# Kernel tuning notes

Measured on AMD Instinct MI355X. Metric: run time of the kernel, lower is better.

The kernel has to match this reference:

```python
import jax, jax.numpy as jnp
import numpy as np

N = 100000      # nodes
E = 3200000     # edges (avg degree 32)
F_IN = 11       # QM9 node feature dim
H = 32          # hidden dim (hard-coded in module)
C = 16          # num_classes


def setup_inputs() -> dict:
    key = jax.random.key(0)
    ks = jax.random.split(key, 8)
    x = jax.random.normal(ks[0], (N, F_IN), jnp.float32)
    edge_index = jax.random.randint(ks[1], (2, E), 0, N, dtype=jnp.int32)
    W1 = jax.random.normal(ks[2], (F_IN, H), jnp.float32) / np.sqrt(F_IN)
    b1 = jnp.zeros((H,), jnp.float32)
    W2 = jax.random.normal(ks[3], (H, H), jnp.float32) / np.sqrt(H)
    b2 = jnp.zeros((H,), jnp.float32)
    W3 = jax.random.normal(ks[4], (H, C), jnp.float32) / np.sqrt(H)
    b3 = jnp.zeros((C,), jnp.float32)
    return {"x": x, "edge_index": edge_index, "W1": W1, "b1": b1,
            "W2": W2, "b2": b2, "W3": W3, "b3": b3}


def gcn_conv(x, src, dst, dinv, W, b):
    # PyG GCNConv: x' = D^{-1/2} (A + I) D^{-1/2} (x W) + b
    h = x @ W                                   # [N, out]
    coef = dinv[src] * dinv[dst]                # [E] symmetric norm per edge
    msg = h[src] * coef[:, None]                # gather + scale
    agg = jnp.zeros_like(h).at[dst].add(msg)    # scatter-add to targets
    agg = agg + h * (dinv * dinv)[:, None]      # self-loop contribution
    return agg + b


def reference(x, edge_index, W1, b1, W2, b2, W3, b3):
    src, dst = edge_index[0], edge_index[1]
    n = x.shape[0]
    # degree including self-loop (counted at target node)
    deg = jnp.zeros((n,), x.dtype).at[dst].add(1.0) + 1.0
    dinv = jax.lax.rsqrt(deg)
    h = jax.nn.relu(gcn_conv(x, src, dst, dinv, W1, b1))
    h = jax.nn.relu(gcn_conv(h, src, dst, dinv, W2, b2))
    h = gcn_conv(h, src, dst, dinv, W3, b3)
    return jax.nn.log_softmax(h, axis=1)
```

## Files before the change

### kernel.cpp

```cpp
#include <hip/hip_runtime.h>
#include <hip/hip_bf16.h>

#define FIN 11
#define HD 32
#define NC 16

#define BK_BITS 9
#define BK_NODES 512
#define NB_MAX 196
#define CAPE 18500
#define STAGE_DEPTH 48
#define FLUSH_N 32

using bf16 = __hip_bfloat16;

static __device__ __forceinline__ float b2f(bf16 v) { return __bfloat162float(v); }

static __device__ __forceinline__ unsigned short f2bf_bits(float f) {
    unsigned int x = __float_as_uint(f);
    return (unsigned short)((x + 0x7FFFu + ((x >> 16) & 1u)) >> 16);
}
static __device__ __forceinline__ float bits2f(unsigned short u) {
    return __uint_as_float(((unsigned int)u) << 16);
}

__global__ __launch_bounds__(256) void k_detect(const unsigned int* __restrict__ xw, int* __restrict__ flag,
                                                int* __restrict__ gcur, int nbq) {
    __shared__ int cnt;
    if (threadIdx.x == 0) cnt = 0;
    __syncthreads();
    for (int i = threadIdx.x; i <= nbq; i += 256) gcur[i] = 0;
    int c = 0;
    for (int i = threadIdx.x; i < 1024; i += 256) c += (xw[i] >> 14) & 1;
    atomicAdd(&cnt, c);
    __syncthreads();
    if (threadIdx.x == 0) *flag = (cnt > 256) ? 1 : 0;
}

__global__ __launch_bounds__(256) void k_binA(const int* __restrict__ ei, int ne, int nb, int per,
                                              int* __restrict__ gcur, unsigned int* __restrict__ bout) {
    __shared__ unsigned int stage[NB_MAX][STAGE_DEPTH];
    __shared__ int cnt[NB_MAX];
    for (int i = threadIdx.x; i < nb; i += 256) cnt[i] = 0;
    __syncthreads();
    int e0 = blockIdx.x * per;
    int e1 = min(e0 + per, ne);
    const int* eis = ei;
    const int* eid = ei + ne;
    for (int base = e0; base < e1; base += 1024) {
#pragma unroll
        for (int k = 0; k < 4; k++) {
            int e = base + k * 256 + threadIdx.x;
            if (e < e1) {
                int s = eis[e], d = eid[e];
                int b = d >> BK_BITS;
                unsigned int pk = ((unsigned int)s << BK_BITS) | (unsigned int)(d & (BK_NODES - 1));
                if (b < nb) {
                    int slot = atomicAdd(&cnt[b], 1);
                    if (slot < STAGE_DEPTH) {
                        stage[b][slot] = pk;
                    } else {
                        atomicSub(&cnt[b], 1);
                        int pos = atomicAdd(&gcur[b], 1);
                        if (pos < CAPE) bout[(size_t)b * CAPE + pos] = pk;
                    }
                }
            }
        }
        __syncthreads();
        if (threadIdx.x < (unsigned)nb) {
            int t = threadIdx.x;
            while (cnt[t] >= FLUSH_N) {
                int pos = atomicAdd(&gcur[t], FLUSH_N);
                if (pos + FLUSH_N <= CAPE) {
                    unsigned int* dstp = bout + (size_t)t * CAPE + pos;
#pragma unroll
                    for (int i = 0; i < FLUSH_N; i++) dstp[i] = stage[t][i];
                }
                int rem = cnt[t] - FLUSH_N;
                for (int i = 0; i < rem; i++) stage[t][i] = stage[t][FLUSH_N + i];
                cnt[t] = rem;
            }
        }
        __syncthreads();
    }
    if (threadIdx.x < (unsigned)nb) {
        int t = threadIdx.x;
        int c = cnt[t];
        if (c > 0) {
            int pos = atomicAdd(&gcur[t], c);
            for (int i = 0; i < c; i++)
                if (pos + i < CAPE) bout[(size_t)t * CAPE + pos + i] = stage[t][i];
        }
    }
}

__global__ __launch_bounds__(256) void k_binB(const unsigned int* __restrict__ bout,
                                              const int* __restrict__ gcur,
                                              float* __restrict__ dinv, int* __restrict__ rowptr,
                                              int* __restrict__ csr, int nn, int nb) {
    __shared__ unsigned int csrimg[CAPE];
    __shared__ int hist[BK_NODES];
    __shared__ int cur[BK_NODES];
    __shared__ int sred[256];
    __shared__ int sbase;
    int b = blockIdx.x;
    {
        int accb = 0, acct = 0;
        for (int i = threadIdx.x; i < nb; i += 256) {
            int v = min(gcur[i], CAPE);
            if (i < b) accb += v;
            acct += v;
        }
        sred[threadIdx.x] = accb;
        __syncthreads();
        for (int off = 128; off > 0; off >>= 1) {
            if (threadIdx.x < off) sred[threadIdx.x] += sred[threadIdx.x + off];
            __syncthreads();
        }
        if (threadIdx.x == 0) sbase = sred[0];
        __syncthreads();
        if (b == 0) {
            sred[threadIdx.x] = acct;
            __syncthreads();
            for (int off = 128; off > 0; off >>= 1) {
                if (threadIdx.x < off) sred[threadIdx.x] += sred[threadIdx.x + off];
                __syncthreads();
            }
            if (threadIdx.x == 0) rowptr[nn] = sred[0];
            __syncthreads();
        }
    }
    int n0 = b << BK_BITS;
    int nval = min(BK_NODES, nn - n0);
    int cnt = min(gcur[b], CAPE);
    int base = sbase;
    const unsigned int* src = bout + (size_t)b * CAPE;
    for (int i = threadIdx.x; i < BK_NODES; i += 256) hist[i] = 0;
    __syncthreads();
    for (int i = threadIdx.x; i < cnt; i += 256)
        atomicAdd(&hist[src[i] & (BK_NODES - 1)], 1);
    __syncthreads();
    for (int i = threadIdx.x; i < nval; i += 256)
        dinv[n0 + i] = rsqrtf((float)hist[i] + 1.0f);
    for (int i = threadIdx.x; i < BK_NODES; i += 256) cur[i] = hist[i];
    __syncthreads();
    for (int off = 1; off < BK_NODES; off <<= 1) {
        int i0 = threadIdx.x, i1 = threadIdx.x + 256;
        int v0 = (i0 >= off) ? cur[i0 - off] : 0;
        int v1 = (i1 >= off) ? cur[i1 - off] : 0;
        __syncthreads();
        cur[i0] += v0;
        cur[i1] += v1;
        __syncthreads();
    }
    for (int i = threadIdx.x; i < BK_NODES; i += 256) {
        int excl = cur[i] - hist[i];
        if (i < nval) rowptr[n0 + i] = base + excl;
        cur[i] = excl;
    }
    __syncthreads();
    for (int i = threadIdx.x; i < cnt; i += 256) {
        unsigned int pk = src[i];
        int l = pk & (BK_NODES - 1);
        int pos = atomicAdd(&cur[l], 1);
        if (pos < CAPE) csrimg[pos] = pk >> BK_BITS;
    }
    __syncthreads();
    for (int i = threadIdx.x; i < cnt; i += 256)
        csr[base + i] = (int)csrimg[i];
}

__global__ __launch_bounds__(256) void k_mm1(const void* __restrict__ xv, const void* __restrict__ Wv,
                                             const int* __restrict__ flag, const float* __restrict__ dinv,
                                             unsigned short* __restrict__ hs, int nn) {
    __shared__ float sW[FIN * HD];
    bool f32 = (*flag != 0);
    if (f32) {
        const float* W = (const float*)Wv;
        for (int i = threadIdx.x; i < FIN * HD; i += blockDim.x) sW[i] = W[i];
    } else {
        const bf16* W = (const bf16*)Wv;
        for (int i = threadIdx.x; i < FIN * HD; i += blockDim.x) sW[i] = b2f(W[i]);
    }
    __syncthreads();
    int t = blockIdx.x * blockDim.x + threadIdx.x;
    int n = t >> 5, j = t & 31;
    if (n >= nn) return;
    float xr[FIN];
    if (f32) {
        const float* p = (const float*)xv + (size_t)n * FIN;
#pragma unroll
        for (int k = 0; k < FIN; k++) xr[k] = p[k];
    } else {
        const bf16* p = (const bf16*)xv + (size_t)n * FIN;
#pragma unroll
        for (int k = 0; k < FIN; k++) xr[k] = b2f(p[k]);
    }
    float acc = 0.0f;
#pragma unroll
    for (int k = 0; k < FIN; k++) acc += xr[k] * sW[k * HD + j];
    hs[(size_t)n * HD + j] = f2bf_bits(acc * dinv[n]);
}

__global__ __launch_bounds__(256) void k_mm2(const void* __restrict__ Wv, const int* __restrict__ flag,
                                             const float* __restrict__ dinv, const float* __restrict__ agg,
                                             unsigned short* __restrict__ hs, int nn) {
    __shared__ float sW[HD * HD];
    __shared__ float sIn[8 * HD];
    bool f32 = (*flag != 0);
    if (f32) {
        const float* W = (const float*)Wv;
        for (int i = threadIdx.x; i < HD * HD; i += blockDim.x) sW[i] = W[i];
    } else {
        const bf16* W = (const bf16*)Wv;
        for (int i = threadIdx.x; i < HD * HD; i += blockDim.x) sW[i] = b2f(W[i]);
    }
    int r0 = blockIdx.x * 8;
    {
        size_t idx = (size_t)r0 * HD + threadIdx.x;
        if (idx < (size_t)nn * HD) {
            float v = agg[idx];
            sIn[threadIdx.x] = v > 0.0f ? v : 0.0f;
        }
    }
    __syncthreads();
    int n = r0 + (threadIdx.x >> 5), j = threadIdx.x & 31;
    if (n >= nn) return;
    const float* r = sIn + (threadIdx.x >> 5) * HD;
    float acc = 0.0f;
#pragma unroll
    for (int k = 0; k < HD; k++) acc += r[k] * sW[k * HD + j];
    hs[(size_t)n * HD + j] = f2bf_bits(acc * dinv[n]);
}

__global__ __launch_bounds__(256) void k_mm3(const void* __restrict__ Wv, const int* __restrict__ flag,
                                             const float* __restrict__ dinv, const float* __restrict__ agg,
                                             unsigned short* __restrict__ hs3, int nn) {
    __shared__ float sW[HD * NC];
    __shared__ float sIn[16 * HD];
    bool f32 = (*flag != 0);
    if (f32) {
        const float* W = (const float*)Wv;
        for (int i = threadIdx.x; i < HD * NC; i += blockDim.x) sW[i] = W[i];
    } else {
        const bf16* W = (const bf16*)Wv;
        for (int i = threadIdx.x; i < HD * NC; i += blockDim.x) sW[i] = b2f(W[i]);
    }
    int r0 = blockIdx.x * 16;
#pragma unroll
    for (int u = 0; u < 2; u++) {
        size_t idx = (size_t)r0 * HD + u * 256 + threadIdx.x;
        if (idx < (size_t)nn * HD) {
            float v = agg[idx];
            sIn[u * 256 + threadIdx.x] = v > 0.0f ? v : 0.0f;
        }
    }
    __syncthreads();
    int n = r0 + (threadIdx.x >> 4), j = threadIdx.x & 15;
    if (n >= nn) return;
    const float* r = sIn + (threadIdx.x >> 4) * HD;
    float acc = 0.0f;
#pragma unroll
    for (int k = 0; k < HD; k++) acc += r[k] * sW[k * NC + j];
    hs3[(size_t)n * NC + j] = f2bf_bits(acc * dinv[n]);
}

__global__ __launch_bounds__(256) void k_g32(const int* __restrict__ rowptr, const int* __restrict__ csr,
                                             const float* __restrict__ dinv, const unsigned short* __restrict__ hs,
                                             const void* __restrict__ bv, const int* __restrict__ flag,
                                             float* __restrict__ agg, int nn) {
    __shared__ float sb[HD];
    bool f32 = (*flag != 0);
    if (threadIdx.x < HD)
        sb[threadIdx.x] = f32 ? ((const float*)bv)[threadIdx.x] : b2f(((const bf16*)bv)[threadIdx.x]);
    __syncthreads();
    int node = blockIdx.x * 4 + (threadIdx.x >> 6);
    if (node >= nn) return;
    int lane = threadIdx.x & 63;
    int g = lane >> 3, q = lane & 7;
    int rs = rowptr[node], re = rowptr[node + 1];
    int deg = re - rs;
    float a0 = 0.0f, a1 = 0.0f, a2 = 0.0f, a3 = 0.0f;
    if (g == 0) {
        uint2 hv = *(const uint2*)(hs + (size_t)node * HD + q * 4);
        a0 = bits2f((unsigned short)(hv.x & 0xFFFFu));
        a1 = bits2f((unsigned short)(hv.x >> 16));
        a2 = bits2f((unsigned short)(hv.y & 0xFFFFu));
        a3 = bits2f((unsigned short)(hv.y >> 16));
    }
    for (int k0 = 0; k0 < deg; k0 += 64) {
        int nk = min(64, deg - k0);
        int myidx = (lane < nk) ? csr[rs + k0 + lane] : 0;
        for (int k = g; k < nk; k += 8) {
            int s = __shfl(myidx, k);
            uint2 hv = *(const uint2*)(hs + (size_t)s * HD + q * 4);
            a0 += bits2f((unsigned short)(hv.x & 0xFFFFu));
            a1 += bits2f((unsigned short)(hv.x >> 16));
            a2 += bits2f((unsigned short)(hv.y & 0xFFFFu));
            a3 += bits2f((unsigned short)(hv.y >> 16));
        }
    }
#pragma unroll
    for (int off = 8; off < 64; off <<= 1) {
        a0 += __shfl_xor(a0, off);
        a1 += __shfl_xor(a1, off);
        a2 += __shfl_xor(a2, off);
        a3 += __shfl_xor(a3, off);
    }
    if (g == 0) {
        float di = dinv[node];
        float4 o = make_float4(di * a0 + sb[q * 4 + 0], di * a1 + sb[q * 4 + 1],
                               di * a2 + sb[q * 4 + 2], di * a3 + sb[q * 4 + 3]);
        *(float4*)(agg + (size_t)node * HD + q * 4) = o;
    }
}

__global__ __launch_bounds__(256) void k_g16lsm(const int* __restrict__ rowptr, const int* __restrict__ csr,
                                                const float* __restrict__ dinv, const unsigned short* __restrict__ hs,
                                                const void* __restrict__ bv, const int* __restrict__ flag,
                                                void* __restrict__ outv, int nn) {
    __shared__ float sb[NC];
    bool f32 = (*flag != 0);
    if (threadIdx.x < NC)
        sb[threadIdx.x] = f32 ? ((const float*)bv)[threadIdx.x] : b2f(((const bf16*)bv)[threadIdx.x]);
    __syncthreads();
    int node = blockIdx.x * 4 + (threadIdx.x >> 6);
    if (node >= nn) return;
    int lane = threadIdx.x & 63;
    int g = lane >> 2, q = lane & 3;
    int rs = rowptr[node], re = rowptr[node + 1];
    int deg = re - rs;
    float a0 = 0.0f, a1 = 0.0f, a2 = 0.0f, a3 = 0.0f;
    if (g == 0) {
        uint2 hv = *(const uint2*)(hs + (size_t)node * NC + q * 4);
        a0 = bits2f((unsigned short)(hv.x & 0xFFFFu));
        a1 = bits2f((unsigned short)(hv.x >> 16));
        a2 = bits2f((unsigned short)(hv.y & 0xFFFFu));
        a3 = bits2f((unsigned short)(hv.y >> 16));
    }
    for (int k0 = 0; k0 < deg; k0 += 64) {
        int nk = min(64, deg - k0);
        int myidx = (lane < nk) ? csr[rs + k0 + lane] : 0;
        for (int k = g; k < nk; k += 16) {
            int s = __shfl(myidx, k);
            uint2 hv = *(const uint2*)(hs + (size_t)s * NC + q * 4);
            a0 += bits2f((unsigned short)(hv.x & 0xFFFFu));
            a1 += bits2f((unsigned short)(hv.x >> 16));
            a2 += bits2f((unsigned short)(hv.y & 0xFFFFu));
            a3 += bits2f((unsigned short)(hv.y >> 16));
        }
    }
#pragma unroll
    for (int off = 4; off < 64; off <<= 1) {
        a0 += __shfl_xor(a0, off);
        a1 += __shfl_xor(a1, off);
        a2 += __shfl_xor(a2, off);
        a3 += __shfl_xor(a3, off);
    }
    if (g == 0) {
        float di = dinv[node];
        float v0 = di * a0 + sb[q * 4 + 0];
        float v1 = di * a1 + sb[q * 4 + 1];
        float v2 = di * a2 + sb[q * 4 + 2];
        float v3 = di * a3 + sb[q * 4 + 3];
        float m = fmaxf(fmaxf(v0, v1), fmaxf(v2, v3));
        m = fmaxf(m, __shfl_xor(m, 1));
        m = fmaxf(m, __shfl_xor(m, 2));
        float s = __expf(v0 - m) + __expf(v1 - m) + __expf(v2 - m) + __expf(v3 - m);
        s += __shfl_xor(s, 1);
        s += __shfl_xor(s, 2);
        float lse = m + __logf(s);
        if (f32) {
            float4 o = make_float4(v0 - lse, v1 - lse, v2 - lse, v3 - lse);
            *(float4*)((float*)outv + (size_t)node * NC + q * 4) = o;
        } else {
            unsigned int lo = f2bf_bits(v0 - lse) | ((unsigned int)f2bf_bits(v1 - lse) << 16);
            unsigned int hi = f2bf_bits(v2 - lse) | ((unsigned int)f2bf_bits(v3 - lse) << 16);
            uint2 o = make_uint2(lo, hi);
            *(uint2*)((unsigned short*)outv + (size_t)node * NC + q * 4) = o;
        }
    }
}

extern "C" void kernel_launch(void* const* d_in, const int* in_sizes, int n_in,
                              void* d_out, int out_size, void* d_ws, size_t ws_size,
                              hipStream_t stream) {
    const void* x  = d_in[0];
    const int*  ei = (const int*)d_in[1];
    const void* W1 = d_in[2];
    const void* b1 = d_in[3];
    const void* W2 = d_in[4];
    const void* b2 = d_in[5];
    const void* W3 = d_in[6];
    const void* b3 = d_in[7];

    const int nn = in_sizes[0] / FIN;
    const int ne = in_sizes[1] / 2;
    const int nb = (nn + BK_NODES - 1) / BK_NODES;

    char* ws = (char*)d_ws;
    size_t off = 0;
    auto carve = [&](size_t bytes) { void* p = ws + off; off += (bytes + 511) & ~(size_t)511; return p; };
    int*            flag   = (int*)carve(4);
    float*          dinv   = (float*)carve((size_t)nn * 4);
    int*            gcur   = (int*)carve((size_t)(nb + 1) * 4);
    int*            rowptr = (int*)carve((size_t)(nn + 1) * 4);
    int*            csr    = (int*)carve((size_t)ne * 4);
    unsigned short* hs     = (unsigned short*)carve((size_t)nn * HD * 2);
    size_t boutB = (size_t)nb * CAPE * 4;
    size_t aggB  = (size_t)nn * HD * 4;
    void* big = carve(boutB > aggB ? boutB : aggB);
    unsigned int* bout = (unsigned int*)big;
    float*        agg  = (float*)big;

    const int B = 256;
    const int gNH  = ((size_t)nn * HD + B - 1) / B;
    const int gR8  = (nn + 7) / 8;
    const int gR16 = (nn + 15) / 16;
    const int gW4  = (nn + 3) / 4;
    const int gridA = 1024;
    const int per   = (ne + gridA - 1) / gridA;

    hipLaunchKernelGGL(k_detect, dim3(1), dim3(B), 0, stream, (const unsigned int*)x, flag, gcur, nb);

    hipLaunchKernelGGL(k_binA, dim3(gridA), dim3(B), 0, stream, ei, ne, nb, per, gcur, bout);
    hipLaunchKernelGGL(k_binB, dim3(nb), dim3(B), 0, stream, bout, gcur, dinv, rowptr, csr, nn, nb);

    hipLaunchKernelGGL(k_mm1, dim3(gNH), dim3(B), 0, stream, x, W1, flag, dinv, hs, nn);
    hipLaunchKernelGGL(k_g32, dim3(gW4), dim3(B), 0, stream, rowptr, csr, dinv, hs, b1, flag, agg, nn);

    hipLaunchKernelGGL(k_mm2, dim3(gR8), dim3(B), 0, stream, W2, flag, dinv, agg, hs, nn);
    hipLaunchKernelGGL(k_g32, dim3(gW4), dim3(B), 0, stream, rowptr, csr, dinv, hs, b2, flag, agg, nn);

    hipLaunchKernelGGL(k_mm3, dim3(gR16), dim3(B), 0, stream, W3, flag, dinv, agg, hs, nn);
    hipLaunchKernelGGL(k_g16lsm, dim3(gW4), dim3(B), 0, stream, rowptr, csr, dinv, hs, b3, flag, d_out, nn);
}
```

Measured before the change: 349.9 us.

## Fuse next-layer dense transform into gather aggregation kernels

The per-layer gather kernels now apply bias and ReLU, then multiply the aggregated row by the next layer's weight matrix in-register via wave shuffles, writing the bf16 pre-scaled features directly. This removes the separate mm2/mm3 kernels and the fp32 agg round-trip through global memory, along with two launches. The fused epilogue adds shuffle and LDS work per node and ping-pongs between two bf16 buffers, one of which aliases the binning scratch.

```diff
diff --git a/kernel.cpp b/kernel.cpp
--- a/kernel.cpp
+++ b/kernel.cpp
@@ -203,77 +203,23 @@
     hs[(size_t)n * HD + j] = f2bf_bits(acc * dinv[n]);
 }
 
-__global__ __launch_bounds__(256) void k_mm2(const void* __restrict__ Wv, const int* __restrict__ flag,
-                                             const float* __restrict__ dinv, const float* __restrict__ agg,
-                                             unsigned short* __restrict__ hs, int nn) {
+__global__ __launch_bounds__(256) void k_gf32(const int* __restrict__ rowptr, const int* __restrict__ csr,
+                                              const float* __restrict__ dinv, const unsigned short* __restrict__ hs,
+                                              const void* __restrict__ bv, const void* __restrict__ Wv,
+                                              const int* __restrict__ flag,
+                                              unsigned short* __restrict__ hout, int nn) {
     __shared__ float sW[HD * HD];
-    __shared__ float sIn[8 * HD];
+    __shared__ float sb[HD];
     bool f32 = (*flag != 0);
     if (f32) {
-        const float* W = (const float*)Wv;
-        for (int i = threadIdx.x; i < HD * HD; i += blockDim.x) sW[i] = W[i];
+        const float* W = (const float*)Wv; const float* b = (const float*)bv;
+        for (int i = threadIdx.x; i < HD * HD; i += 256) sW[i] = W[i];
+        if (threadIdx.x < HD) sb[threadIdx.x] = b[threadIdx.x];
     } else {
-        const bf16* W = (const bf16*)Wv;
-        for (int i = threadIdx.x; i < HD * HD; i += blockDim.x) sW[i] = b2f(W[i]);
-    }
-    int r0 = blockIdx.x * 8;
-    {
-        size_t idx = (size_t)r0 * HD + threadIdx.x;
-        if (idx < (size_t)nn * HD) {
-            float v = agg[idx];
-            sIn[threadIdx.x] = v > 0.0f ? v : 0.0f;
-        }
-    }
-    __syncthreads();
-    int n = r0 + (threadIdx.x >> 5), j = threadIdx.x & 31;
-    if (n >= nn) return;
-    const float* r = sIn + (threadIdx.x >> 5) * HD;
-    float acc = 0.0f;
-#pragma unroll
-    for (int k = 0; k < HD; k++) acc += r[k] * sW[k * HD + j];
-    hs[(size_t)n * HD + j] = f2bf_bits(acc * dinv[n]);
-}
-
-__global__ __launch_bounds__(256) void k_mm3(const void* __restrict__ Wv, const int* __restrict__ flag,
-                                             const float* __restrict__ dinv, const float* __restrict__ agg,
-                                             unsigned short* __restrict__ hs3, int nn) {
-    __shared__ float sW[HD * NC];
-    __shared__ float sIn[16 * HD];
-    bool f32 = (*flag != 0);
-    if (f32) {
-        const float* W = (const float*)Wv;
-        for (int i = threadIdx.x; i < HD * NC; i += blockDim.x) sW[i] = W[i];
-    } else {
-        const bf16* W = (const bf16*)Wv;
-        for (int i = threadIdx.x; i < HD * NC; i += blockDim.x) sW[i] = b2f(W[i]);
-    }
-    int r0 = blockIdx.x * 16;
-#pragma unroll
-    for (int u = 0; u < 2; u++) {
-        size_t idx = (size_t)r0 * HD + u * 256 + threadIdx.x;
-        if (idx < (size_t)nn * HD) {
-            float v = agg[idx];
-            sIn[u * 256 + threadIdx.x] = v > 0.0f ? v : 0.0f;
-        }
-    }
-    __syncthreads();
-    int n = r0 + (threadIdx.x >> 4), j = threadIdx.x & 15;
-    if (n >= nn) return;
-    const float* r = sIn + (threadIdx.x >> 4) * HD;
-    float acc = 0.0f;
-#pragma unroll
-    for (int k = 0; k < HD; k++) acc += r[k] * sW[k * NC + j];
-    hs3[(size_t)n * NC + j] = f2bf_bits(acc * dinv[n]);
-}
-
-__global__ __launch_bounds__(256) void k_g32(const int* __restrict__ rowptr, const int* __restrict__ csr,
-                                             const float* __restrict__ dinv, const unsigned short* __restrict__ hs,
-                                             const void* __restrict__ bv, const int* __restrict__ flag,
-                                             float* __restrict__ agg, int nn) {
-    __shared__ float sb[HD];
-    bool f32 = (*flag != 0);
-    if (threadIdx.x < HD)
-        sb[threadIdx.x] = f32 ? ((const float*)bv)[threadIdx.x] : b2f(((const bf16*)bv)[threadIdx.x]);
+        const bf16* W = (const bf16*)Wv; const bf16* b = (const bf16*)bv;
+        for (int i = threadIdx.x; i < HD * HD; i += 256) sW[i] = b2f(W[i]);
+        if (threadIdx.x < HD) sb[threadIdx.x] = b2f(b[threadIdx.x]);
+    }
     __syncthreads();
     int node = blockIdx.x * 4 + (threadIdx.x >> 6);
     if (node >= nn) return;
@@ -308,12 +254,89 @@
         a2 += __shfl_xor(a2, off);
         a3 += __shfl_xor(a3, off);
     }
+    float di = dinv[node];
+    float rr[4];
+    rr[0] = fmaxf(di * a0 + sb[q * 4 + 0], 0.0f);
+    rr[1] = fmaxf(di * a1 + sb[q * 4 + 1], 0.0f);
+    rr[2] = fmaxf(di * a2 + sb[q * 4 + 2], 0.0f);
+    rr[3] = fmaxf(di * a3 + sb[q * 4 + 3], 0.0f);
+    int j = lane & 31;
+    float acc = 0.0f;
+#pragma unroll
+    for (int k = 0; k < HD; k++) {
+        float rk = __shfl(rr[k & 3], (lane & 56) | (k >> 2));
+        acc += rk * sW[k * HD + j];
+    }
+    if (lane < HD)
+        hout[(size_t)node * HD + lane] = f2bf_bits(acc * di);
+}
+
+__global__ __launch_bounds__(256) void k_gfo(const int* __restrict__ rowptr, const int* __restrict__ csr,
+                                             const float* __restrict__ dinv, const unsigned short* __restrict__ hs,
+                                             const void* __restrict__ bv, const void* __restrict__ Wv,
+                                             const int* __restrict__ flag,
+                                             unsigned short* __restrict__ hout, int nn) {
+    __shared__ float sW[HD * NC];
+    __shared__ float sb[HD];
+    bool f32 = (*flag != 0);
+    if (f32) {
+        const float* W = (const float*)Wv; const float* b = (const float*)bv;
+        for (int i = threadIdx.x; i < HD * NC; i += 256) sW[i] = W[i];
+        if (threadIdx.x < HD) sb[threadIdx.x] = b[threadIdx.x];
+    } else {
+        const bf16* W = (const bf16*)Wv; const bf16* b = (const bf16*)bv;
+        for (int i = threadIdx.x; i < HD * NC; i += 256) sW[i] = b2f(W[i]);
+        if (threadIdx.x < HD) sb[threadIdx.x] = b2f(b[threadIdx.x]);
+    }
+    __syncthreads();
+    int node = blockIdx.x * 4 + (threadIdx.x >> 6);
+    if (node >= nn) return;
+    int lane = threadIdx.x & 63;
+    int g = lane >> 3, q = lane & 7;
+    int rs = rowptr[node], re = rowptr[node + 1];
+    int deg = re - rs;
+    float a0 = 0.0f, a1 = 0.0f, a2 = 0.0f, a3 = 0.0f;
     if (g == 0) {
-        float di = dinv[node];
-        float4 o = make_float4(di * a0 + sb[q * 4 + 0], di * a1 + sb[q * 4 + 1],
-                               di * a2 + sb[q * 4 + 2], di * a3 + sb[q * 4 + 3]);
-        *(float4*)(agg + (size_t)node * HD + q * 4) = o;
-    }
+        uint2 hv = *(const uint2*)(hs + (size_t)node * HD + q * 4);
+        a0 = bits2f((unsigned short)(hv.x & 0xFFFFu));
+        a1 = bits2f((unsigned short)(hv.x >> 16));
+        a2 = bits2f((unsigned short)(hv.y & 0xFFFFu));
+        a3 = bits2f((unsigned short)(hv.y >> 16));
+    }
+    for (int k0 = 0; k0 < deg; k0 += 64) {
+        int nk = min(64, deg - k0);
+        int myidx = (lane < nk) ? csr[rs + k0 + lane] : 0;
+        for (int k = g; k < nk; k += 8) {
+            int s = __shfl(myidx, k);
+            uint2 hv = *(const uint2*)(hs + (size_t)s * HD + q * 4);
+            a0 += bits2f((unsigned short)(hv.x & 0xFFFFu));
+            a1 += bits2f((unsigned short)(hv.x >> 16));
+            a2 += bits2f((unsigned short)(hv.y & 0xFFFFu));
+            a3 += bits2f((unsigned short)(hv.y >> 16));
+        }
+    }
+#pragma unroll
+    for (int off = 8; off < 64; off <<= 1) {
+        a0 += __shfl_xor(a0, off);
+        a1 += __shfl_xor(a1, off);
+        a2 += __shfl_xor(a2, off);
+        a3 += __shfl_xor(a3, off);
+    }
+    float di = dinv[node];
+    float rr[4];
+    rr[0] = fmaxf(di * a0 + sb[q * 4 + 0], 0.0f);
+    rr[1] = fmaxf(di * a1 + sb[q * 4 + 1], 0.0f);
+    rr[2] = fmaxf(di * a2 + sb[q * 4 + 2], 0.0f);
+    rr[3] = fmaxf(di * a3 + sb[q * 4 + 3], 0.0f);
+    int j = lane & (NC - 1);
+    float acc = 0.0f;
+#pragma unroll
+    for (int k = 0; k < HD; k++) {
+        float rk = __shfl(rr[k & 3], (lane & 56) | (k >> 2));
+        acc += rk * sW[k * NC + j];
+    }
+    if (lane < NC)
+        hout[(size_t)node * NC + lane] = f2bf_bits(acc * di);
 }
 
 __global__ __launch_bounds__(256) void k_g16lsm(const int* __restrict__ rowptr, const int* __restrict__ csr,
@@ -407,17 +430,16 @@
     int*            gcur   = (int*)carve((size_t)(nb + 1) * 4);
     int*            rowptr = (int*)carve((size_t)(nn + 1) * 4);
     int*            csr    = (int*)carve((size_t)ne * 4);
-    unsigned short* hs     = (unsigned short*)carve((size_t)nn * HD * 2);
+    unsigned short* hs_a   = (unsigned short*)carve((size_t)nn * HD * 2);
     size_t boutB = (size_t)nb * CAPE * 4;
-    size_t aggB  = (size_t)nn * HD * 4;
-    void* big = carve(boutB > aggB ? boutB : aggB);
-    unsigned int* bout = (unsigned int*)big;
-    float*        agg  = (float*)big;
+    size_t hsB   = (size_t)nn * HD * 2;
+    void* big = carve(boutB > hsB ? boutB : hsB);
+    unsigned int*   bout = (unsigned int*)big;
+    unsigned short* hs_b = (unsigned short*)big;
+    unsigned short* hs3  = hs_a;
 
     const int B = 256;
     const int gNH  = ((size_t)nn * HD + B - 1) / B;
-    const int gR8  = (nn + 7) / 8;
-    const int gR16 = (nn + 15) / 16;
     const int gW4  = (nn + 3) / 4;
     const int gridA = 1024;
     const int per   = (ne + gridA - 1) / gridA;
@@ -427,12 +449,8 @@
     hipLaunchKernelGGL(k_binA, dim3(gridA), dim3(B), 0, stream, ei, ne, nb, per, gcur, bout);
     hipLaunchKernelGGL(k_binB, dim3(nb), dim3(B), 0, stream, bout, gcur, dinv, rowptr, csr, nn, nb);
 
-    hipLaunchKernelGGL(k_mm1, dim3(gNH), dim3(B), 0, stream, x, W1, flag, dinv, hs, nn);
-    hipLaunchKernelGGL(k_g32, dim3(gW4), dim3(B), 0, stream, rowptr, csr, dinv, hs, b1, flag, agg, nn);
-
-    hipLaunchKernelGGL(k_mm2, dim3(gR8), dim3(B), 0, stream, W2, flag, dinv, agg, hs, nn);
-    hipLaunchKernelGGL(k_g32, dim3(gW4), dim3(B), 0, stream, rowptr, csr, dinv, hs, b2, flag, agg, nn);
-
-    hipLaunchKernelGGL(k_mm3, dim3(gR16), dim3(B), 0, stream, W3, flag, dinv, agg, hs, nn);
-    hipLaunchKernelGGL(k_g16lsm, dim3(gW4), dim3(B), 0, stream, rowptr, csr, dinv, hs, b3, flag, d_out, nn);
-}
+    hipLaunchKernelGGL(k_mm1, dim3(gNH), dim3(B), 0, stream, x, W1, flag, dinv, hs_a, nn);
+    hipLaunchKernelGGL(k_gf32, dim3(gW4), dim3(B), 0, stream, rowptr, csr, dinv, hs_a, b1, W2, flag, hs_b, nn);
+    hipLaunchKernelGGL(k_gfo, dim3(gW4), dim3(B), 0, stream, rowptr, csr, dinv, hs_b, b2, W3, flag, hs3, nn);
+    hipLaunchKernelGGL(k_g16lsm, dim3(gW4), dim3(B), 0, stream, rowptr, csr, dinv, hs3, b3, flag, d_out, nn);
+}
```

After: 380.3 us. +8.7%, slower.
